# Performance work log

Hardware: AMD Instinct MI355X
Metric: run time of the kernel (lower is better)

## Reference

```python
import jax, jax.numpy as jnp
import numpy as np

NUM_IN_CH = 64
DIM = 256
HEADS = 8


def conv1x1(x, w):
    # x: [b,c,h,w], w: [o,c,1,1] -> [b,o,h,w]
    return jnp.einsum('bchw,oc->bohw', x, w[:, :, 0, 0])


def dwconv3(x, w):
    # depthwise 3x3, padding=1; w: [c,1,3,3]
    return jax.lax.conv_general_dilated(
        x, w, window_strides=(1, 1), padding='SAME',
        feature_group_count=x.shape[1],
        dimension_numbers=('NCHW', 'OIHW', 'NCHW'))


def setup_inputs() -> dict:
    key = jax.random.key(0)
    ks = jax.random.split(key, 12)
    B, C, H, W = 8, NUM_IN_CH, 128, 128
    s = 0.02
    return {
        'x': jax.random.normal(ks[0], (B, C, H, W), jnp.float32),
        'y': jax.random.normal(ks[1], (B, C, H, W), jnp.float32),
        'z': jax.random.normal(ks[2], (B, C, H, W), jnp.float32),
        'Wq': jax.random.normal(ks[3], (DIM, C, 1, 1), jnp.float32) * s,
        'Wq_dw': jax.random.normal(ks[4], (DIM, 1, 3, 3), jnp.float32) * s,
        'Wk': jax.random.normal(ks[5], (DIM, C, 1, 1), jnp.float32) * s,
        'Wk_dw': jax.random.normal(ks[6], (DIM, 1, 3, 3), jnp.float32) * s,
        'Wv': jax.random.normal(ks[7], (DIM, C, 1, 1), jnp.float32) * s,
        'Wv_dw': jax.random.normal(ks[8], (DIM, 1, 3, 3), jnp.float32) * s,
        'Wproj': jax.random.normal(ks[9], (DIM, DIM, 1, 1), jnp.float32) * s,
        'Wfus': jax.random.normal(ks[10], (DIM, 3 * C, 1, 1), jnp.float32) * s,
        'temperature': jnp.ones((HEADS, 1, 1), jnp.float32),
    }


def reference(x, y, z, Wq, Wq_dw, Wk, Wk_dw, Wv, Wv_dw, Wproj, Wfus, temperature):
    b, c, h, w = x.shape
    hw = h * w
    q = dwconv3(conv1x1(x, Wq), Wq_dw)
    k = dwconv3(conv1x1(y, Wk), Wk_dw)
    v = dwconv3(conv1x1(z, Wv), Wv_dw)
    f = conv1x1(jnp.concatenate([x, y, z], axis=1), Wfus)

    def to_heads(t):  # [b, dim, h, w] -> [b, head, c_head, hw]
        return t.reshape(b, HEADS, DIM // HEADS, hw)

    q, k, v = to_heads(q), to_heads(k), to_heads(v)
    # L2-normalize over the spatial (hw) axis, eps matches torch F.normalize
    qn = q / jnp.maximum(jnp.sqrt(jnp.sum(q * q, axis=-1, keepdims=True)), 1e-12)
    kn = k / jnp.maximum(jnp.sqrt(jnp.sum(k * k, axis=-1, keepdims=True)), 1e-12)
    attn = jnp.einsum('bhcn,bhdn->bhcd', qn, kn) * temperature  # [b,head,c,c]
    attn = jax.nn.softmax(attn, axis=-1)
    out = jnp.einsum('bhcd,bhdn->bhcn', attn, v).reshape(b, DIM, h, w)
    out = conv1x1(out, Wproj)
    return out + f
```

## Files before the change

### kernel.cpp

```cpp
#include <hip/hip_runtime.h>
#include <cstdint>

#define B_   8
#define CIN  64
#define DIM_ 256
#define H_   128
#define W_   128
#define HW_  (H_*W_)

typedef unsigned short u16;
typedef unsigned int   u32;
typedef short short8 __attribute__((ext_vector_type(8)));
typedef float f32x4  __attribute__((ext_vector_type(4)));

__device__ __forceinline__ u16 f2bf(float f) {
    u32 u = __float_as_uint(f);
    u32 r = (u + 0x7fffu + ((u >> 16) & 1u)) >> 16;
    return (u16)r;
}
__device__ __forceinline__ float bf2f(u16 h) {
    return __uint_as_float(((u32)h) << 16);
}

__global__ __launch_bounds__(512, 6) void convdw_kernel(
    const float* __restrict__ in, const float* __restrict__ Wc,
    const float* __restrict__ Wd, u16* __restrict__ dst)
{
    __shared__ u16 Wtc[2][32 * 64];
    __shared__ u16 Xt[192 * 64];
    __shared__ u16 Pt[32 * 196];
    __shared__ float wlds[9 * 36];

    const int tid = threadIdx.x;
    const int tile = blockIdx.x;
    const int b = blockIdx.y;
    const int y0 = (tile >> 3) * 8;
    const int x0 = (tile & 7) * 16;

    {
        const int row = tid >> 4, seg = tid & 15;
        float4 f = *(const float4*)(Wc + (size_t)row * 64 + seg * 4);
        uint2 pk;
        pk.x = f2bf(f.x) | ((u32)f2bf(f.y) << 16);
        pk.y = f2bf(f.z) | ((u32)f2bf(f.w) << 16);
        *(uint2*)&Wtc[0][row * 64 + ((seg * 4) ^ ((row & 7) << 3))] = pk;
    }
    {
        const float* inb = in + (size_t)b * CIN * HW_;
        for (int i = tid; i < 1440; i += 512) {
            int chg = i / 180;
            int px = i - chg * 180;
            int py = px / 18;
            int pxi = px - py * 18;
            int gy = y0 - 1 + py, gx = x0 - 1 + pxi;
            uint4 pk = make_uint4(0, 0, 0, 0);
            if (gy >= 0 && gy < H_ && gx >= 0 && gx < W_) {
                const float* sp = inb + (size_t)(chg * 8) * HW_ + (size_t)gy * W_ + gx;
                u32 wv[4];
                #pragma unroll
                for (int j = 0; j < 4; ++j) {
                    float a = sp[(size_t)(2 * j) * HW_];
                    float c = sp[(size_t)(2 * j + 1) * HW_];
                    wv[j] = f2bf(a) | ((u32)f2bf(c) << 16);
                }
                pk = make_uint4(wv[0], wv[1], wv[2], wv[3]);
            }
            *(uint4*)&Xt[px * 64 + ((chg * 8) ^ ((px & 7) << 3))] = pk;
        }
    }
    __syncthreads();

    const int lane = tid & 63, w = tid >> 6;
    const int g = lane >> 4, ln = lane & 15;
    const int wm = w & 1;
    const int wpar = w >> 1;

    u16* db = dst + (size_t)b * DIM_ * HW_;

    for (int c = 0; c < 8; ++c) {
        const int cb = c & 1;
        f32x4 acc[3];
        #pragma unroll
        for (int jj = 0; jj < 3; ++jj) acc[jj] = (f32x4){0.f, 0.f, 0.f, 0.f};
        short8 af[2];
        {
            int m = wm * 16 + ln;
            af[0] = *(const short8*)&Wtc[cb][m * 64 + ((g * 8) ^ ((m & 7) << 3))];
            af[1] = *(const short8*)&Wtc[cb][m * 64 + ((32 + g * 8) ^ ((m & 7) << 3))];
        }
        #pragma unroll
        for (int jj = 0; jj < 3; ++jj) {
            int j = jj * 4 + wpar;
            int px = j * 16 + ln;
            #pragma unroll
            for (int ks = 0; ks < 2; ++ks) {
                short8 bf = *(const short8*)&Xt[px * 64 + ((ks * 32 + g * 8) ^ ((px & 7) << 3))];
                acc[jj] = __builtin_amdgcn_mfma_f32_16x16x32_bf16(af[ks], bf, acc[jj], 0, 0, 0);
            }
        }

        if (c < 7) {
            const int row = tid >> 4, seg = tid & 15;
            float4 f = *(const float4*)(Wc + (size_t)((c + 1) * 32 + row) * 64 + seg * 4);
            uint2 pk;
            pk.x = f2bf(f.x) | ((u32)f2bf(f.y) << 16);
            pk.y = f2bf(f.z) | ((u32)f2bf(f.w) << 16);
            *(uint2*)&Wtc[cb ^ 1][row * 64 + ((seg * 4) ^ ((row & 7) << 3))] = pk;
        }

        #pragma unroll
        for (int jj = 0; jj < 3; ++jj) {
            int j = jj * 4 + wpar;
            int px = j * 16 + ln;
            #pragma unroll
            for (int r = 0; r < 4; ++r)
                Pt[(wm * 16 + g * 4 + r) * 196 + px] = f2bf(acc[jj][r]);
        }
        for (int i = tid; i < 288; i += 512) {
            int ch = i / 9, tap = i - ch * 9;
            wlds[tap * 36 + ch] = Wd[(size_t)(c * 32 + ch) * 9 + tap];
        }
        __syncthreads();

        {
            const int chl = tid >> 4;
            const int sub = tid & 15;
            const int oy = sub >> 1, ox0 = (sub & 1) * 8;
            float wr[9];
            #pragma unroll
            for (int t = 0; t < 9; ++t) wr[t] = wlds[t * 36 + chl];
            const u32* pw = (const u32*)&Pt[chl * 196];
            float R[3][10];
            #pragma unroll
            for (int dy = 0; dy < 3; ++dy) {
                int wbase = (oy + dy) * 9 + (ox0 >> 1);
                #pragma unroll
                for (int u = 0; u < 5; ++u) {
                    u32 wrd = pw[wbase + u];
                    R[dy][2 * u]     = bf2f((u16)wrd);
                    R[dy][2 * u + 1] = bf2f((u16)(wrd >> 16));
                }
            }
            float o[8];
            #pragma unroll
            for (int i = 0; i < 8; ++i) {
                float s = R[0][i] * wr[0];
                s = fmaf(R[0][i + 1], wr[1], s);
                s = fmaf(R[0][i + 2], wr[2], s);
                s = fmaf(R[1][i],     wr[3], s);
                s = fmaf(R[1][i + 1], wr[4], s);
                s = fmaf(R[1][i + 2], wr[5], s);
                s = fmaf(R[2][i],     wr[6], s);
                s = fmaf(R[2][i + 1], wr[7], s);
                s = fmaf(R[2][i + 2], wr[8], s);
                o[i] = s;
            }
            uint4 pk;
            pk.x = f2bf(o[0]) | ((u32)f2bf(o[1]) << 16);
            pk.y = f2bf(o[2]) | ((u32)f2bf(o[3]) << 16);
            pk.z = f2bf(o[4]) | ((u32)f2bf(o[5]) << 16);
            pk.w = f2bf(o[6]) | ((u32)f2bf(o[7]) << 16);
            *(uint4*)(db + (size_t)(c * 32 + chl) * HW_ + (size_t)(y0 + oy) * W_ + x0 + ox0) = pk;
        }
        if (c < 7) __syncthreads();
    }
}

__global__ __launch_bounds__(256) void gram_mfma_kernel(
    const u16* __restrict__ q, const u16* __restrict__ k,
    float* __restrict__ pgram, float* __restrict__ pssq, float* __restrict__ pssk)
{
    __shared__ float red[4][1024];
    __shared__ float redq[4][32];
    __shared__ float redk[4][32];

    const int bh = blockIdx.y;
    const int chunk = blockIdx.x;
    const int tid = threadIdx.x;
    const int lane = tid & 63, wid = tid >> 6;
    const int g = lane >> 4, ln = lane & 15;

    const size_t off = (size_t)(bh * 32 + ln) * HW_ + chunk * 2048 + wid * 512 + g * 8;
    const u16* qp = q + off;
    const u16* kp = k + off;

    f32x4 aqk[2][2] = {};
    f32x4 aqq[2] = {};
    f32x4 akk[2] = {};

    #pragma unroll 4
    for (int n = 0; n < 512; n += 32) {
        short8 qf[2], kf[2];
        qf[0] = *(const short8*)(qp + n);
        qf[1] = *(const short8*)(qp + (size_t)16 * HW_ + n);
        kf[0] = *(const short8*)(kp + n);
        kf[1] = *(const short8*)(kp + (size_t)16 * HW_ + n);
        #pragma unroll
        for (int ti = 0; ti < 2; ++ti)
            #pragma unroll
            for (int tj = 0; tj < 2; ++tj)
                aqk[ti][tj] = __builtin_amdgcn_mfma_f32_16x16x32_bf16(qf[ti], kf[tj], aqk[ti][tj], 0, 0, 0);
        #pragma unroll
        for (int ti = 0; ti < 2; ++ti) {
            aqq[ti] = __builtin_amdgcn_mfma_f32_16x16x32_bf16(qf[ti], qf[ti], aqq[ti], 0, 0, 0);
            akk[ti] = __builtin_amdgcn_mfma_f32_16x16x32_bf16(kf[ti], kf[ti], akk[ti], 0, 0, 0);
        }
    }

    #pragma unroll
    for (int ti = 0; ti < 2; ++ti)
        #pragma unroll
        for (int tj = 0; tj < 2; ++tj)
            #pragma unroll
            for (int r = 0; r < 4; ++r)
                red[wid][(ti * 16 + g * 4 + r) * 32 + tj * 16 + ln] = aqk[ti][tj][r];
    if ((ln >> 2) == g) {
        #pragma unroll
        for (int ti = 0; ti < 2; ++ti) {
            redq[wid][ti * 16 + ln] = aqq[ti][ln & 3];
            redk[wid][ti * 16 + ln] = akk[ti][ln & 3];
        }
    }
    __syncthreads();

    for (int p = tid; p < 1024; p += 256) {
        float s = red[0][p] + red[1][p] + red[2][p] + red[3][p];
        pgram[((size_t)bh * 8 + chunk) * 1024 + p] = s;
    }
    if (tid < 32) {
        pssq[((size_t)bh * 8 + chunk) * 32 + tid] =
            redq[0][tid] + redq[1][tid] + redq[2][tid] + redq[3][tid];
    } else if (tid < 64) {
        int j = tid & 31;
        pssk[((size_t)bh * 8 + chunk) * 32 + j] =
            redk[0][j] + redk[1][j] + redk[2][j] + redk[3][j];
    }
}

__global__ __launch_bounds__(256) void softproj_kernel(
    const float* __restrict__ pgram, const float* __restrict__ pssq,
    const float* __restrict__ pssk, const float* __restrict__ Wproj,
    const float* __restrict__ temp, u16* __restrict__ Amm)
{
    __shared__ float att[32][33];
    __shared__ float nq[32], nk[32];

    const int bh = blockIdx.x;
    const int h = bh & 7;
    const int b = bh >> 3;
    const int tid = threadIdx.x;

    for (int p = tid; p < 1024; p += 256) {
        float s = 0.f;
        #pragma unroll
        for (int c = 0; c < 8; ++c) s += pgram[((size_t)bh * 8 + c) * 1024 + p];
        att[p >> 5][p & 31] = s;
    }
    if (tid < 32) {
        float s = 0.f;
        #pragma unroll
        for (int c = 0; c < 8; ++c) s += pssq[((size_t)bh * 8 + c) * 32 + tid];
        nq[tid] = fmaxf(sqrtf(s), 1e-12f);
    } else if (tid < 64) {
        int i = tid & 31;
        float s = 0.f;
        #pragma unroll
        for (int c = 0; c < 8; ++c) s += pssk[((size_t)bh * 8 + c) * 32 + i];
        nk[i] = fmaxf(sqrtf(s), 1e-12f);
    }
    __syncthreads();

    const float T = temp[h];
    if (tid < 32) {
        int i = tid;
        float row[32];
        float mx = -1e30f;
        float qi = T / nq[i];
        #pragma unroll
        for (int j = 0; j < 32; ++j) {
            float v = att[i][j] * qi / nk[j];
            row[j] = v;
            mx = fmaxf(mx, v);
        }
        float s = 0.f;
        #pragma unroll
        for (int j = 0; j < 32; ++j) { float e = expf(row[j] - mx); row[j] = e; s += e; }
        float inv = 1.f / s;
        #pragma unroll
        for (int j = 0; j < 32; ++j) att[i][j] = row[j] * inv;
    }
    __syncthreads();

    const int o = tid;
    float wp[32];
    #pragma unroll
    for (int i2 = 0; i2 < 32; i2 += 4)
        *(float4*)&wp[i2] = *(const float4*)&Wproj[(size_t)o * DIM_ + h * 32 + i2];
    u16* arow = Amm + ((size_t)b * DIM_ + o) * DIM_ + h * 32;
    #pragma unroll
    for (int j = 0; j < 32; ++j) {
        float s = 0.f;
        #pragma unroll
        for (int i = 0; i < 32; ++i) s = fmaf(wp[i], att[i][j], s);
        arow[j] = f2bf(s);
    }
}

__global__ __launch_bounds__(256) void wfus_cast_kernel(
    const float* __restrict__ Wfus, u16* __restrict__ Afus)
{
    int idx = blockIdx.x * 256 + threadIdx.x;
    int base = idx * 8;
    float4 f0 = *(const float4*)(Wfus + base);
    float4 f1 = *(const float4*)(Wfus + base + 4);
    uint4 pk;
    pk.x = f2bf(f0.x) | ((u32)f2bf(f0.y) << 16);
    pk.y = f2bf(f0.z) | ((u32)f2bf(f0.w) << 16);
    pk.z = f2bf(f1.x) | ((u32)f2bf(f1.y) << 16);
    pk.w = f2bf(f1.z) | ((u32)f2bf(f1.w) << 16);
    *(uint4*)(Afus + base) = pk;
}

#define LOADB_F4(KC, W) do {                                                    \
    if ((KC) < 4) {                                                             \
        _Pragma("unroll") for (int i_ = 0; i_ < 2; ++i_) {                      \
            const u16* vb_ = vbuf + ((size_t)b * DIM_ + (KC) * 64 + (qq0 + 2 * i_) * 16) * HW_ + px0 + pxu; \
            _Pragma("unroll") for (int jj_ = 0; jj_ < 8; ++jj_)                 \
                W[i_][jj_] = (u32)vb_[(size_t)(2 * jj_) * HW_]                  \
                           | ((u32)vb_[(size_t)(2 * jj_ + 1) * HW_] << 16);     \
        }                                                                       \
    } else {                                                                    \
        const float* bp_ = ((KC) == 4) ? xin : ((KC) == 5) ? yin : zin;         \
        _Pragma("unroll") for (int i_ = 0; i_ < 2; ++i_) {                      \
            const float* sp_ = bp_ + ((size_t)b * CIN + (qq0 + 2 * i_) * 16) * HW_ + px0 + pxu; \
            _Pragma("unroll") for (int jj_ = 0; jj_ < 8; ++jj_)                 \
                W[i_][jj_] = (u32)f2bf(sp_[(size_t)(2 * jj_) * HW_])            \
                           | ((u32)f2bf(sp_[(size_t)(2 * jj_ + 1) * HW_]) << 16); \
        }                                                                       \
    } } while (0)

#define WRITEB_F4(BUF, W) do {                                                  \
    u16* dd_ = &Bl[BUF][pxu * 64];                                              \
    _Pragma("unroll") for (int i_ = 0; i_ < 2; ++i_) {                          \
        int qq_ = qq0 + 2 * i_;                                                 \
        *(uint4*)&dd_[(qq_ * 16)     ^ ((pxu & 7) << 3)] = make_uint4(W[i_][0], W[i_][1], W[i_][2], W[i_][3]); \
        *(uint4*)&dd_[(qq_ * 16 + 8) ^ ((pxu & 7) << 3)] = make_uint4(W[i_][4], W[i_][5], W[i_][6], W[i_][7]); \
    } } while (0)

#define LOADA_F4(KC, A) do {                                                    \
    _Pragma("unroll") for (int ks_ = 0; ks_ < 2; ++ks_)                         \
    _Pragma("unroll") for (int fm_ = 0; fm_ < 2; ++fm_) {                       \
        int m_ = m0 + fm_ * 16 + ln;                                            \
        const u16* ap_ = ((KC) < 4)                                             \
            ? Amm + ((size_t)b * DIM_ + m_) * DIM_ + (KC) * 64 + ks_ * 32 + g * 8 \
            : Afus + (size_t)m_ * 192 + ((KC) - 4) * 64 + ks_ * 32 + g * 8;     \
        A[ks_ * 2 + fm_] = *(const short8*)ap_;                                 \
    } } while (0)

__global__ __launch_bounds__(256, 4) void final4_kernel(
    const u16* __restrict__ Amm, const u16* __restrict__ Afus,
    const u16* __restrict__ vbuf,
    const float* __restrict__ xin, const float* __restrict__ yin,
    const float* __restrict__ zin, float* __restrict__ out)
{
    __shared__ u16 Bl[2][128 * 64];

    const int tid = threadIdx.x;
    const int px0 = blockIdx.x * 128;
    const int o0  = blockIdx.y * 128;
    const int b   = blockIdx.z;
    const int lane = tid & 63, wid = tid >> 6;
    const int g = lane >> 4, ln = lane & 15;
    const int m0 = o0 + wid * 32;
    const int pxu = tid & 127;
    const int qq0 = tid >> 7;

    f32x4 acc[2][8] = {};
    short8 aC[4], aN[4];
    u32 wN[2][8];

    LOADA_F4(0, aC);
    {
        u32 w0[2][8];
        LOADB_F4(0, w0);
        WRITEB_F4(0, w0);
    }
    __syncthreads();
    LOADA_F4(1, aN);
    LOADB_F4(1, wN);

    #pragma unroll
    for (int kc = 0; kc < 7; ++kc) {
        const int cur = kc & 1;

        #pragma unroll
        for (int ks = 0; ks < 2; ++ks)
            #pragma unroll
            for (int fn = 0; fn < 8; ++fn) {
                int p = fn * 16 + ln;
                short8 bf = *(const short8*)&Bl[cur][p * 64 + ((ks * 32 + g * 8) ^ ((p & 7) << 3))];
                acc[0][fn] = __builtin_amdgcn_mfma_f32_16x16x32_bf16(aC[ks * 2 + 0], bf, acc[0][fn], 0, 0, 0);
                acc[1][fn] = __builtin_amdgcn_mfma_f32_16x16x32_bf16(aC[ks * 2 + 1], bf, acc[1][fn], 0, 0, 0);
            }

        if (kc < 6) {
            WRITEB_F4(cur ^ 1, wN);
            __syncthreads();
            #pragma unroll
            for (int r = 0; r < 4; ++r) aC[r] = aN[r];
            if (kc < 5) {
                LOADA_F4(kc + 2, aN);
                LOADB_F4(kc + 2, wN);
            }
        }
    }

    float* op = out + (size_t)b * DIM_ * HW_;
    #pragma unroll
    for (int fm = 0; fm < 2; ++fm)
        #pragma unroll
        for (int fn = 0; fn < 8; ++fn)
            #pragma unroll
            for (int r = 0; r < 4; ++r) {
                int ch = m0 + fm * 16 + g * 4 + r;
                op[(size_t)ch * HW_ + px0 + fn * 16 + ln] = acc[fm][fn][r];
            }
}

extern "C" void kernel_launch(void* const* d_in, const int* in_sizes, int n_in,
                              void* d_out, int out_size, void* d_ws, size_t ws_size,
                              hipStream_t stream) {
    (void)in_sizes; (void)n_in; (void)out_size; (void)ws_size;

    const float* x     = (const float*)d_in[0];
    const float* y     = (const float*)d_in[1];
    const float* z     = (const float*)d_in[2];
    const float* Wq    = (const float*)d_in[3];
    const float* Wqd   = (const float*)d_in[4];
    const float* Wk    = (const float*)d_in[5];
    const float* Wkd   = (const float*)d_in[6];
    const float* Wv    = (const float*)d_in[7];
    const float* Wvd   = (const float*)d_in[8];
    const float* Wproj = (const float*)d_in[9];
    const float* Wfus  = (const float*)d_in[10];
    const float* temp  = (const float*)d_in[11];

    const size_t QELEMS = (size_t)B_ * DIM_ * HW_;

    u16* qbuf = (u16*)d_out + QELEMS;
    u16* kvbuf = (u16*)d_ws;
    char* wsp = (char*)d_ws + QELEMS * sizeof(u16);
    float* pgram = (float*)wsp;                       wsp += 64 * 8 * 1024 * 4;
    float* pssq  = (float*)wsp;                       wsp += 64 * 8 * 32 * 4;
    float* pssk  = (float*)wsp;                       wsp += 64 * 8 * 32 * 4;
    u16*   Amm   = (u16*)wsp;                         wsp += (size_t)B_ * DIM_ * DIM_ * 2;
    u16*   Afus  = (u16*)wsp;

    dim3 fgrid(128, B_);

    wfus_cast_kernel<<<24, 256, 0, stream>>>(Wfus, Afus);
    convdw_kernel<<<fgrid, 512, 0, stream>>>(x, Wq, Wqd, qbuf);
    convdw_kernel<<<fgrid, 512, 0, stream>>>(y, Wk, Wkd, kvbuf);
    gram_mfma_kernel<<<dim3(8, 64), 256, 0, stream>>>(qbuf, kvbuf, pgram, pssq, pssk);
    softproj_kernel<<<64, 256, 0, stream>>>(pgram, pssq, pssk, Wproj, temp, Amm);
    convdw_kernel<<<fgrid, 512, 0, stream>>>(z, Wv, Wvd, kvbuf);
    final4_kernel<<<dim3(128, 2, B_), 256, 0, stream>>>(Amm, Afus, kvbuf, x, y, z, (float*)d_out);
}
```

Before: 266.7 us.

## Compute all output channels per block in final GEMM to share B tiles

```diff
diff --git a/kernel.cpp b/kernel.cpp
--- a/kernel.cpp
+++ b/kernel.cpp
@@ -321,33 +321,27 @@
     *(uint4*)(Afus + base) = pk;
 }
 
-#define LOADB_F4(KC, W) do {                                                    \
+#define LOADB_F8(KC, W) do {                                                    \
     if ((KC) < 4) {                                                             \
-        _Pragma("unroll") for (int i_ = 0; i_ < 2; ++i_) {                      \
-            const u16* vb_ = vbuf + ((size_t)b * DIM_ + (KC) * 64 + (qq0 + 2 * i_) * 16) * HW_ + px0 + pxu; \
-            _Pragma("unroll") for (int jj_ = 0; jj_ < 8; ++jj_)                 \
-                W[i_][jj_] = (u32)vb_[(size_t)(2 * jj_) * HW_]                  \
-                           | ((u32)vb_[(size_t)(2 * jj_ + 1) * HW_] << 16);     \
-        }                                                                       \
+        const u16* vb_ = vbuf + ((size_t)b * DIM_ + (KC) * 64 + qq * 16) * HW_ + px0 + pxu; \
+        _Pragma("unroll") for (int jj_ = 0; jj_ < 8; ++jj_)                     \
+            W[jj_] = (u32)vb_[(size_t)(2 * jj_) * HW_]                          \
+                   | ((u32)vb_[(size_t)(2 * jj_ + 1) * HW_] << 16);             \
     } else {                                                                    \
         const float* bp_ = ((KC) == 4) ? xin : ((KC) == 5) ? yin : zin;         \
-        _Pragma("unroll") for (int i_ = 0; i_ < 2; ++i_) {                      \
-            const float* sp_ = bp_ + ((size_t)b * CIN + (qq0 + 2 * i_) * 16) * HW_ + px0 + pxu; \
-            _Pragma("unroll") for (int jj_ = 0; jj_ < 8; ++jj_)                 \
-                W[i_][jj_] = (u32)f2bf(sp_[(size_t)(2 * jj_) * HW_])            \
-                           | ((u32)f2bf(sp_[(size_t)(2 * jj_ + 1) * HW_]) << 16); \
-        }                                                                       \
+        const float* sp_ = bp_ + ((size_t)b * CIN + qq * 16) * HW_ + px0 + pxu; \
+        _Pragma("unroll") for (int jj_ = 0; jj_ < 8; ++jj_)                     \
+            W[jj_] = (u32)f2bf(sp_[(size_t)(2 * jj_) * HW_])                    \
+                   | ((u32)f2bf(sp_[(size_t)(2 * jj_ + 1) * HW_]) << 16);       \
     } } while (0)
 
-#define WRITEB_F4(BUF, W) do {                                                  \
+#define WRITEB_F8(BUF, W) do {                                                  \
     u16* dd_ = &Bl[BUF][pxu * 64];                                              \
-    _Pragma("unroll") for (int i_ = 0; i_ < 2; ++i_) {                          \
-        int qq_ = qq0 + 2 * i_;                                                 \
-        *(uint4*)&dd_[(qq_ * 16)     ^ ((pxu & 7) << 3)] = make_uint4(W[i_][0], W[i_][1], W[i_][2], W[i_][3]); \
-        *(uint4*)&dd_[(qq_ * 16 + 8) ^ ((pxu & 7) << 3)] = make_uint4(W[i_][4], W[i_][5], W[i_][6], W[i_][7]); \
-    } } while (0)
-
-#define LOADA_F4(KC, A) do {                                                    \
+    *(uint4*)&dd_[(qq * 16)     ^ ((pxu & 7) << 3)] = make_uint4(W[0], W[1], W[2], W[3]); \
+    *(uint4*)&dd_[(qq * 16 + 8) ^ ((pxu & 7) << 3)] = make_uint4(W[4], W[5], W[6], W[7]); \
+    } while (0)
+
+#define LOADA_F8(KC, A) do {                                                    \
     _Pragma("unroll") for (int ks_ = 0; ks_ < 2; ++ks_)                         \
     _Pragma("unroll") for (int fm_ = 0; fm_ < 2; ++fm_) {                       \
         int m_ = m0 + fm_ * 16 + ln;                                            \
@@ -357,7 +351,7 @@
         A[ks_ * 2 + fm_] = *(const short8*)ap_;                                 \
     } } while (0)
 
-__global__ __launch_bounds__(256, 4) void final4_kernel(
+__global__ __launch_bounds__(512, 6) void final8_kernel(
     const u16* __restrict__ Amm, const u16* __restrict__ Afus,
     const u16* __restrict__ vbuf,
     const float* __restrict__ xin, const float* __restrict__ yin,
@@ -367,27 +361,26 @@
 
     const int tid = threadIdx.x;
     const int px0 = blockIdx.x * 128;
-    const int o0  = blockIdx.y * 128;
-    const int b   = blockIdx.z;
+    const int b   = blockIdx.y;
     const int lane = tid & 63, wid = tid >> 6;
     const int g = lane >> 4, ln = lane & 15;
-    const int m0 = o0 + wid * 32;
+    const int m0 = (wid >> 2) * 128 + (wid & 3) * 32;
     const int pxu = tid & 127;
-    const int qq0 = tid >> 7;
+    const int qq  = tid >> 7;
 
     f32x4 acc[2][8] = {};
     short8 aC[4], aN[4];
-    u32 wN[2][8];
-
-    LOADA_F4(0, aC);
+    u32 wN[8];
+
+    LOADA_F8(0, aC);
     {
-        u32 w0[2][8];
-        LOADB_F4(0, w0);
-        WRITEB_F4(0, w0);
+        u32 w0[8];
+        LOADB_F8(0, w0);
+        WRITEB_F8(0, w0);
     }
     __syncthreads();
-    LOADA_F4(1, aN);
-    LOADB_F4(1, wN);
+    LOADA_F8(1, aN);
+    LOADB_F8(1, wN);
 
     #pragma unroll
     for (int kc = 0; kc < 7; ++kc) {
@@ -404,13 +397,13 @@
             }
 
         if (kc < 6) {
-            WRITEB_F4(cur ^ 1, wN);
+            WRITEB_F8(cur ^ 1, wN);
             __syncthreads();
             #pragma unroll
             for (int r = 0; r < 4; ++r) aC[r] = aN[r];
             if (kc < 5) {
-                LOADA_F4(kc + 2, aN);
-                LOADB_F4(kc + 2, wN);
+                LOADA_F8(kc + 2, aN);
+                LOADB_F8(kc + 2, wN);
             }
         }
     }
@@ -464,5 +457,5 @@
     gram_mfma_kernel<<<dim3(8, 64), 256, 0, stream>>>(qbuf, kvbuf, pgram, pssq, pssk);
     softproj_kernel<<<64, 256, 0, stream>>>(pgram, pssq, pssk, Wproj, temp, Amm);
     convdw_kernel<<<fgrid, 512, 0, stream>>>(z, Wv, Wvd, kvbuf);
-    final4_kernel<<<dim3(128, 2, B_), 256, 0, stream>>>(Amm, Afus, kvbuf, x, y, z, (float*)d_out);
-}
+    final8_kernel<<<dim3(128, B_), 512, 0, stream>>>(Amm, Afus, kvbuf, x, y, z, (float*)d_out);
+}
```

Result: slower. 550.1 us (+106.2%).
